# Kernel optimization log

Hardware: AMD Instinct MI355X
Metric: run time of the kernel (lower is better)

Reference implementation:

```python
import jax, jax.numpy as jnp
import numpy as np

N = 4096
IN_DIM = 512
NUM_HEADS = 8
SUB_DIM = 64
ETA = 0.5
LAMBDA_SPARSE = 0.1
EDGE_PROB = 0.01


def setup_inputs() -> dict:
    key = jax.random.key(0)
    k_h, k_u, k_a = jax.random.split(key, 3)
    H = jax.random.normal(k_h, (N, IN_DIM), dtype=jnp.float32)
    # Per-head orthonormal subspace bases (QR init, as in the torch module)
    raw = jax.random.normal(k_u, (NUM_HEADS, IN_DIM, SUB_DIM), dtype=jnp.float32)
    U = jax.vmap(lambda a: jnp.linalg.qr(a)[0])(raw)  # [K, in_dim, r]
    # Binary adjacency mask with self-loops (float 0/1)
    adj = (jax.random.uniform(k_a, (N, N)) < EDGE_PROB).astype(jnp.float32)
    adj_mask = jnp.maximum(adj, jnp.eye(N, dtype=jnp.float32))
    threshold = jnp.full((IN_DIM,), LAMBDA_SPARSE, dtype=jnp.float32)
    return {"H": H, "adj_mask": adj_mask, "U": U, "threshold": threshold}


def reference(H, adj_mask, U, threshold):
    r = U.shape[-1]
    scale = jnp.asarray(r, H.dtype) ** 0.5
    # Z_k = U_k^T H^T  -> [K, r, n]
    Z = jnp.einsum('kdr,nd->krn', U, H)
    # scores[k, i, j] = Z_k[:, i] . Z_k[:, j] / sqrt(r), masked to neighbors
    scores = jnp.einsum('kri,krj->kij', Z, Z) / scale
    scores = scores + (1.0 - adj_mask) * (-1e9)
    alpha = jax.nn.softmax(scores, axis=-1)          # [K, n, n]
    # Z_agg[k, :, i] = sum_j alpha[k, i, j] * Z_k[:, j]
    Z_agg = jnp.einsum('krj,kij->kri', Z, alpha)      # [K, r, n]
    # project back and sum heads: [n, d]
    agg = jnp.einsum('kdr,kri->id', U, Z_agg)
    H_half = H + ETA * agg
    H_out = jax.nn.relu(H_half - threshold[None, :])
    # orthogonality loss: sum_{k<l} ||U_k^T U_l||_F^2
    gram = jnp.einsum('kdr,lds->klrs', U, U)
    sq = jnp.sum(gram ** 2, axis=(-1, -2))            # [K, K]
    orth_loss = 0.5 * (jnp.sum(sq) - jnp.trace(sq))
    return H_out, orth_loss
```

## Files before the change

kernel.cpp:

```cpp
#include <hip/hip_runtime.h>
#include <hip/hip_bf16.h>

#define NN   4096
#define DD   512
#define KH   8
#define RR   64
#define CAP  128

typedef unsigned short u16;
typedef unsigned int   u32;
typedef __attribute__((ext_vector_type(8))) short short8;
typedef __attribute__((ext_vector_type(4))) float f32x4;

__device__ __forceinline__ float bflo(u32 v){ union{u32 i; float f;} c; c.i = v << 16;        return c.f; }
__device__ __forceinline__ float bfhi(u32 v){ union{u32 i; float f;} c; c.i = v & 0xFFFF0000u; return c.f; }
__device__ __forceinline__ u16 f2bf(float f){ __hip_bfloat16 h = __float2bfloat16(f); return *reinterpret_cast<u16*>(&h); }

__global__ __launch_bounds__(256) void prep_scan(const float* __restrict__ H, const float* __restrict__ U,
                                                 const float* __restrict__ adj,
                                                 u16* __restrict__ Hb, u16* __restrict__ Bt1,
                                                 u16* __restrict__ Bt2,
                                                 int* __restrict__ nlist, int* __restrict__ cnt,
                                                 float* __restrict__ lossA, int* __restrict__ doneA) {
    __shared__ float tile[64][65];
    __shared__ int   list[CAP];
    __shared__ int   cntS;
    const int b = blockIdx.x, t = threadIdx.x;
    if (b < 4096) {
        const int i = b;
        if (t == 0) cntS = 0;
        __syncthreads();
        const float* arow = adj + (size_t)i * NN;
        #pragma unroll
        for (int qq = 0; qq < 4; qq++) {
            int j = (qq * 256 + t) * 4;
            float4 mv = *(const float4*)(arow + j);
            if (mv.x != 0.f) { int p = atomicAdd(&cntS, 1); if (p < CAP) list[p] = j;     }
            if (mv.y != 0.f) { int p = atomicAdd(&cntS, 1); if (p < CAP) list[p] = j + 1; }
            if (mv.z != 0.f) { int p = atomicAdd(&cntS, 1); if (p < CAP) list[p] = j + 2; }
            if (mv.w != 0.f) { int p = atomicAdd(&cntS, 1); if (p < CAP) list[p] = j + 3; }
        }
        __syncthreads();
        const int n = min(cntS, CAP);
        if (t < n) nlist[(size_t)i * CAP + t] = list[t];
        if (t == 0) cnt[i] = n;
        return;
    }
    if (b < 6144) {
        size_t id = (size_t)(b - 4096) * 256 + t;
        float4 v = *(const float4*)(H + id * 4);
        ushort4 o; o.x = f2bf(v.x); o.y = f2bf(v.y); o.z = f2bf(v.z); o.w = f2bf(v.w);
        *(ushort4*)(Hb + id * 4) = o;
        return;
    }
    if (b == 6208) { if (t == 0) { lossA[0] = 0.f; doneA[0] = 0; } return; }
    const int b2 = b - 6144;
    const int k = b2 >> 3, d0 = (b2 & 7) * 64;
    #pragma unroll
    for (int s = 0; s < 4; s++) {
        int u = t + 256 * s;
        int dd = u >> 4, rq = u & 15;
        float4 v = *(const float4*)(U + ((size_t)(k * DD + d0 + dd)) * RR + rq * 4);
        tile[dd][rq * 4 + 0] = v.x; tile[dd][rq * 4 + 1] = v.y;
        tile[dd][rq * 4 + 2] = v.z; tile[dd][rq * 4 + 3] = v.w;
    }
    __syncthreads();
    {   int r = t >> 2;
        #pragma unroll
        for (int ii = 0; ii < 16; ii++) {
            int dd = (t & 3) * 16 + ii;
            Bt1[(size_t)(k * RR + r) * DD + d0 + dd] = f2bf(tile[dd][r]);
        }
    }
    {   int dd = t >> 2, rb = (t & 3) * 16;
        #pragma unroll
        for (int ii = 0; ii < 16; ii++) {
            Bt2[(size_t)(d0 + dd) * DD + k * RR + rb + ii] = f2bf(tile[dd][rb + ii]);
        }
    }
}

__global__ __launch_bounds__(256) void zgemm_mfma(const u16* __restrict__ Hb, const u16* __restrict__ Bt1,
                                                  u16* __restrict__ Zb) {
    __shared__ short As[64][72];
    __shared__ short Bs[64][72];
    const int t = threadIdx.x;
    const int i0 = blockIdx.x * 64, n0 = blockIdx.y * 64;
    const int w = t >> 6, lane = t & 63;
    const int lm = lane & 15, lg = lane >> 4;
    f32x4 acc[4] = {};
    for (int kc = 0; kc < DD; kc += 64) {
        #pragma unroll
        for (int s = 0; s < 2; s++) {
            int c = t + 256 * s; int row = c >> 3, g = c & 7;
            *(short8*)&As[row][g * 8] = *(const short8*)(Hb  + (size_t)(i0 + row) * DD + kc + g * 8);
            *(short8*)&Bs[row][g * 8] = *(const short8*)(Bt1 + (size_t)(n0 + row) * DD + kc + g * 8);
        }
        __syncthreads();
        #pragma unroll
        for (int ks = 0; ks < 64; ks += 32) {
            short8 af = *(const short8*)&As[w * 16 + lm][ks + lg * 8];
            #pragma unroll
            for (int b = 0; b < 4; b++) {
                short8 bfr = *(const short8*)&Bs[b * 16 + lm][ks + lg * 8];
                acc[b] = __builtin_amdgcn_mfma_f32_16x16x32_bf16(af, bfr, acc[b], 0, 0, 0);
            }
        }
        __syncthreads();
    }
    #pragma unroll
    for (int b = 0; b < 4; b++)
        #pragma unroll
        for (int q = 0; q < 4; q++) {
            int row = i0 + w * 16 + lg * 4 + q;
            int col = n0 + b * 16 + lm;
            Zb[(size_t)row * DD + col] = f2bf(acc[b][q]);
        }
}

__global__ __launch_bounds__(512) void attn7(const u16* __restrict__ Zb, const int* __restrict__ nlist,
                                             const int* __restrict__ cnt, u16* __restrict__ Zaggb) {
    const int i = blockIdx.x, t = threadIdx.x;
    const int k = t >> 6, lane = t & 63;
    __shared__ int   nbrS[CAP + 16];
    __shared__ float ziS[DD];
    __shared__ u32   zbufU[KH][16][36];
    __shared__ float wS[KH][16];
    const int ci = cnt[i];
    for (int u = t; u < ci; u += 512) nbrS[u] = nlist[(size_t)i * CAP + u];
    if (t < 256) {
        u32 v = *(const u32*)(Zb + (size_t)i * DD + t * 2);
        ziS[t * 2] = bflo(v); ziS[t * 2 + 1] = bfhi(v);
    }
    __syncthreads();
    if (t < 16) nbrS[ci + t] = nbrS[0];
    __syncthreads();

    const int n = lane >> 2, q = lane & 3;
    const int half = lane >> 5, L = lane & 31;
    const float4* zi4 = (const float4*)(ziS + k * 64 + q * 16);
    float m = -3.0e38f, l = 0.f, accA = 0.f, accB = 0.f;

    for (int base = 0; base < ci; base += 16) {
        const int cact = min(16, ci - base);
        const int j = nbrS[base + n];
        const uint4* zp = (const uint4*)(Zb + (size_t)j * DD + k * 64 + q * 16);
        uint4 v0 = zp[0], v1 = zp[1];
        *(uint4*)&zbufU[k][n][q * 8]     = v0;
        *(uint4*)&zbufU[k][n][q * 8 + 4] = v1;
        float4 a0 = zi4[0], a1 = zi4[1], a2 = zi4[2], a3 = zi4[3];
        float s = bflo(v0.x)*a0.x + bfhi(v0.x)*a0.y + bflo(v0.y)*a0.z + bfhi(v0.y)*a0.w
                + bflo(v0.z)*a1.x + bfhi(v0.z)*a1.y + bflo(v0.w)*a1.z + bfhi(v0.w)*a1.w
                + bflo(v1.x)*a2.x + bfhi(v1.x)*a2.y + bflo(v1.y)*a2.z + bfhi(v1.y)*a2.w
                + bflo(v1.z)*a3.x + bfhi(v1.z)*a3.y + bflo(v1.w)*a3.z + bfhi(v1.w)*a3.w;
        s += __shfl_xor(s, 1);
        s += __shfl_xor(s, 2);
        s *= 0.125f;
        if (n >= cact) s = -3.0e38f;
        float mx = s;
        #pragma unroll
        for (int off = 4; off < 64; off <<= 1) mx = fmaxf(mx, __shfl_xor(mx, off));
        const float mnew = fmaxf(m, mx);
        const float scale = __expf(m - mnew);
        const float e = (n < cact) ? __expf(s - mnew) : 0.f;
        float se = e;
        #pragma unroll
        for (int off = 4; off < 64; off <<= 1) se += __shfl_xor(se, off);
        l = l * scale + se;
        m = mnew;
        accA *= scale; accB *= scale;
        if (q == 0) wS[k][n] = e;
        __syncthreads();
        for (int c = half; c < cact; c += 2) {
            const float wgt = wS[k][c];
            u32 z2 = zbufU[k][c][L];
            accA += wgt * bflo(z2);
            accB += wgt * bfhi(z2);
        }
        __syncthreads();
    }
    accA += __shfl_xor(accA, 32);
    accB += __shfl_xor(accB, 32);
    if (lane < 32) {
        const float inv = 1.0f / l;
        u32 o = ((u32)f2bf(accA * inv)) | (((u32)f2bf(accB * inv)) << 16);
        *(u32*)(Zaggb + (size_t)i * DD + k * 64 + 2 * L) = o;
    }
}

__global__ __launch_bounds__(256) void outgemm_mfma(const u16* __restrict__ Ab, const u16* __restrict__ Btb,
                                                    const float* __restrict__ H, const float* __restrict__ thr,
                                                    float* __restrict__ out) {
    __shared__ short As[64][72];
    __shared__ short Bs[64][72];
    const int t = threadIdx.x;
    const int i0 = blockIdx.x * 64, n0 = blockIdx.y * 64;
    const int w = t >> 6, lane = t & 63;
    const int lm = lane & 15, lg = lane >> 4;
    f32x4 acc[4] = {};
    for (int kc = 0; kc < DD; kc += 64) {
        #pragma unroll
        for (int s = 0; s < 2; s++) {
            int c = t + 256 * s; int row = c >> 3, g = c & 7;
            *(short8*)&As[row][g * 8] = *(const short8*)(Ab  + (size_t)(i0 + row) * DD + kc + g * 8);
            *(short8*)&Bs[row][g * 8] = *(const short8*)(Btb + (size_t)(n0 + row) * DD + kc + g * 8);
        }
        __syncthreads();
        #pragma unroll
        for (int ks = 0; ks < 64; ks += 32) {
            short8 af = *(const short8*)&As[w * 16 + lm][ks + lg * 8];
            #pragma unroll
            for (int b = 0; b < 4; b++) {
                short8 bfr = *(const short8*)&Bs[b * 16 + lm][ks + lg * 8];
                acc[b] = __builtin_amdgcn_mfma_f32_16x16x32_bf16(af, bfr, acc[b], 0, 0, 0);
            }
        }
        __syncthreads();
    }
    #pragma unroll
    for (int b = 0; b < 4; b++) {
        const int col = n0 + b * 16 + lm;
        const float th = thr[col];
        #pragma unroll
        for (int q = 0; q < 4; q++) {
            int row = i0 + w * 16 + lg * 4 + q;
            float h = H[(size_t)row * DD + col];
            out[(size_t)row * DD + col] = fmaxf(h + 0.5f * acc[b][q] - th, 0.f);
        }
    }
}

__global__ __launch_bounds__(256) void orth_kernel(const float* __restrict__ U, float* __restrict__ loss,
                                                   int* __restrict__ done, float* __restrict__ outLoss) {
    __shared__ float UkT[64][20];
    __shared__ float UlT[64][68];
    const int pb = blockIdx.x >> 2, strip = blockIdx.x & 3;
    int idx = pb, k = 0, lh = 1;
    #pragma unroll
    for (int kk = 0; kk < 8; kk++) {
        int c = 7 - kk;
        if (idx < c) { k = kk; lh = kk + 1 + idx; break; }
        idx -= c;
    }
    const int t = threadIdx.x;
    const int r = t & 15;
    const int s0 = (t >> 4) * 4;
    const int r0g = strip * 16;
    const float* Uk = U + (size_t)k  * DD * RR;
    const float* Ul = U + (size_t)lh * DD * RR;
    float a0 = 0.f, a1 = 0.f, a2 = 0.f, a3 = 0.f;
    for (int dc = 0; dc < DD; dc += 64) {
        {   int dd = t >> 2, rq = t & 3;
            *(float4*)&UkT[dd][rq * 4] = *(const float4*)(Uk + (size_t)(dc + dd) * RR + r0g + rq * 4);
        }
        #pragma unroll
        for (int s = 0; s < 4; s++) {
            int u = t + 256 * s;
            int dd = u >> 4, sq = u & 15;
            *(float4*)&UlT[dd][sq * 4] = *(const float4*)(Ul + (size_t)(dc + dd) * RR + sq * 4);
        }
        __syncthreads();
        #pragma unroll 4
        for (int dd = 0; dd < 64; dd++) {
            float a = UkT[dd][r];
            float4 bv = *(const float4*)&UlT[dd][s0];
            a0 += a * bv.x; a1 += a * bv.y; a2 += a * bv.z; a3 += a * bv.w;
        }
        __syncthreads();
    }
    float v = a0 * a0 + a1 * a1 + a2 * a2 + a3 * a3;
    #pragma unroll
    for (int off = 32; off; off >>= 1) v += __shfl_down(v, off, 64);
    __shared__ float red[4];
    if ((t & 63) == 0) red[t >> 6] = v;
    __syncthreads();
    if (t == 0) {
        atomicAdd(loss, red[0] + red[1] + red[2] + red[3]);
        __threadfence();
        int d = atomicAdd(done, 1);
        if (d == 111) {
            float total = atomicAdd(loss, 0.f);
            outLoss[0] = total;
        }
    }
}

extern "C" void kernel_launch(void* const* d_in, const int* in_sizes, int n_in,
                              void* d_out, int out_size, void* d_ws, size_t ws_size,
                              hipStream_t stream) {
    const float* H   = (const float*)d_in[0];
    const float* adj = (const float*)d_in[1];
    const float* U   = (const float*)d_in[2];
    const float* thr = (const float*)d_in[3];
    float* out = (float*)d_out;

    char* ws = (char*)d_ws;
    float* lossA = (float*)ws;
    int*   doneA = (int*)(ws + 64);
    u16*   Hb    = (u16*)(ws + 1024);
    u16*   Zb    = (u16*)(ws + 1024 + 4u * 1024 * 1024);
    u16*   Zaggb = (u16*)(ws + 1024 + 8u * 1024 * 1024);
    u16*   Bt1   = (u16*)(ws + 1024 + 12u * 1024 * 1024);
    u16*   Bt2   = (u16*)(ws + 1024 + 12u * 1024 * 1024 + 512u * 1024);
    int*   nlist = (int*)(ws + 1024 + 13u * 1024 * 1024);
    int*   cnt   = (int*)(ws + 1024 + 15u * 1024 * 1024 + 512u * 1024);

    prep_scan<<<6209, 256, 0, stream>>>(H, U, adj, Hb, Bt1, Bt2, nlist, cnt, lossA, doneA);
    zgemm_mfma<<<dim3(64, 8), 256, 0, stream>>>(Hb, Bt1, Zb);
    attn7<<<NN, 512, 0, stream>>>(Zb, nlist, cnt, Zaggb);
    outgemm_mfma<<<dim3(64, 8), 256, 0, stream>>>(Zaggb, Bt2, H, thr, out);
    orth_kernel<<<112, 256, 0, stream>>>(U, lossA, doneA, out + (size_t)NN * DD);
}
```

Before: 174.9 us.

## Keep attention accumulation in registers and drop shared-memory staging and barriers

The sparse attention kernel no longer stages neighbor rows, weights, query vector and neighbor list in LDS. Each lane keeps its 16-element slice of the query and a 16-float accumulator in registers, rescales it online, and the lanes are combined with a butterfly shuffle reduction once at the end. This removes two __syncthreads per 16-neighbor chunk and the LDS traffic. In exchange it uses more registers and adds a 16-wide shuffle reduction at the end.

```diff
diff --git a/kernel.cpp b/kernel.cpp
--- a/kernel.cpp
+++ b/kernel.cpp
@@ -118,41 +118,41 @@
         }
 }
 
-__global__ __launch_bounds__(512) void attn7(const u16* __restrict__ Zb, const int* __restrict__ nlist,
+__global__ __launch_bounds__(512) void attn8(const u16* __restrict__ Zb, const int* __restrict__ nlist,
                                              const int* __restrict__ cnt, u16* __restrict__ Zaggb) {
     const int i = blockIdx.x, t = threadIdx.x;
     const int k = t >> 6, lane = t & 63;
-    __shared__ int   nbrS[CAP + 16];
-    __shared__ float ziS[DD];
-    __shared__ u32   zbufU[KH][16][36];
-    __shared__ float wS[KH][16];
+    const int n = lane >> 2, q = lane & 3;
     const int ci = cnt[i];
-    for (int u = t; u < ci; u += 512) nbrS[u] = nlist[(size_t)i * CAP + u];
-    if (t < 256) {
-        u32 v = *(const u32*)(Zb + (size_t)i * DD + t * 2);
-        ziS[t * 2] = bflo(v); ziS[t * 2 + 1] = bfhi(v);
-    }
-    __syncthreads();
-    if (t < 16) nbrS[ci + t] = nbrS[0];
-    __syncthreads();
-
-    const int n = lane >> 2, q = lane & 3;
-    const int half = lane >> 5, L = lane & 31;
-    const float4* zi4 = (const float4*)(ziS + k * 64 + q * 16);
-    float m = -3.0e38f, l = 0.f, accA = 0.f, accB = 0.f;
+    const int* nl = nlist + (size_t)i * CAP;
+
+    float a[16];
+    {
+        const uint4* zp = (const uint4*)(Zb + (size_t)i * DD + k * 64 + q * 16);
+        uint4 w0 = zp[0], w1 = zp[1];
+        a[0] = bflo(w0.x); a[1] = bfhi(w0.x); a[2]  = bflo(w0.y); a[3]  = bfhi(w0.y);
+        a[4] = bflo(w0.z); a[5] = bfhi(w0.z); a[6]  = bflo(w0.w); a[7]  = bfhi(w0.w);
+        a[8] = bflo(w1.x); a[9] = bfhi(w1.x); a[10] = bflo(w1.y); a[11] = bfhi(w1.y);
+        a[12]= bflo(w1.z); a[13]= bfhi(w1.z); a[14] = bflo(w1.w); a[15] = bfhi(w1.w);
+    }
+
+    float m = -3.0e38f, l = 0.f;
+    float acc[16] = {};
 
     for (int base = 0; base < ci; base += 16) {
         const int cact = min(16, ci - base);
-        const int j = nbrS[base + n];
+        const int idx = (n < cact) ? base + n : 0;
+        const int j = nl[idx];
         const uint4* zp = (const uint4*)(Zb + (size_t)j * DD + k * 64 + q * 16);
         uint4 v0 = zp[0], v1 = zp[1];
-        *(uint4*)&zbufU[k][n][q * 8]     = v0;
-        *(uint4*)&zbufU[k][n][q * 8 + 4] = v1;
-        float4 a0 = zi4[0], a1 = zi4[1], a2 = zi4[2], a3 = zi4[3];
-        float s = bflo(v0.x)*a0.x + bfhi(v0.x)*a0.y + bflo(v0.y)*a0.z + bfhi(v0.y)*a0.w
-                + bflo(v0.z)*a1.x + bfhi(v0.z)*a1.y + bflo(v0.w)*a1.z + bfhi(v0.w)*a1.w
-                + bflo(v1.x)*a2.x + bfhi(v1.x)*a2.y + bflo(v1.y)*a2.z + bfhi(v1.y)*a2.w
-                + bflo(v1.z)*a3.x + bfhi(v1.z)*a3.y + bflo(v1.w)*a3.z + bfhi(v1.w)*a3.w;
+        float zf[16];
+        zf[0] = bflo(v0.x); zf[1] = bfhi(v0.x); zf[2]  = bflo(v0.y); zf[3]  = bfhi(v0.y);
+        zf[4] = bflo(v0.z); zf[5] = bfhi(v0.z); zf[6]  = bflo(v0.w); zf[7]  = bfhi(v0.w);
+        zf[8] = bflo(v1.x); zf[9] = bfhi(v1.x); zf[10] = bflo(v1.y); zf[11] = bfhi(v1.y);
+        zf[12]= bflo(v1.z); zf[13]= bfhi(v1.z); zf[14] = bflo(v1.w); zf[15] = bfhi(v1.w);
+        float s = 0.f;
+        #pragma unroll
+        for (int d = 0; d < 16; d++) s += zf[d] * a[d];
         s += __shfl_xor(s, 1);
         s += __shfl_xor(s, 2);
         s *= 0.125f;
@@ -168,23 +168,22 @@
         for (int off = 4; off < 64; off <<= 1) se += __shfl_xor(se, off);
         l = l * scale + se;
         m = mnew;
-        accA *= scale; accB *= scale;
-        if (q == 0) wS[k][n] = e;
-        __syncthreads();
-        for (int c = half; c < cact; c += 2) {
-            const float wgt = wS[k][c];
-            u32 z2 = zbufU[k][c][L];
-            accA += wgt * bflo(z2);
-            accB += wgt * bfhi(z2);
-        }
-        __syncthreads();
-    }
-    accA += __shfl_xor(accA, 32);
-    accB += __shfl_xor(accB, 32);
-    if (lane < 32) {
+        #pragma unroll
+        for (int d = 0; d < 16; d++) acc[d] = acc[d] * scale + e * zf[d];
+    }
+    #pragma unroll
+    for (int off = 4; off < 64; off <<= 1)
+        #pragma unroll
+        for (int d = 0; d < 16; d++) acc[d] += __shfl_xor(acc[d], off);
+    if (n == 0) {
         const float inv = 1.0f / l;
-        u32 o = ((u32)f2bf(accA * inv)) | (((u32)f2bf(accB * inv)) << 16);
-        *(u32*)(Zaggb + (size_t)i * DD + k * 64 + 2 * L) = o;
+        u32 o[8];
+        #pragma unroll
+        for (int p = 0; p < 8; p++)
+            o[p] = ((u32)f2bf(acc[2 * p] * inv)) | (((u32)f2bf(acc[2 * p + 1] * inv)) << 16);
+        uint4* dst = (uint4*)(Zaggb + (size_t)i * DD + k * 64 + q * 16);
+        dst[0] = make_uint4(o[0], o[1], o[2], o[3]);
+        dst[1] = make_uint4(o[4], o[5], o[6], o[7]);
     }
 }
 
@@ -307,7 +306,7 @@
 
     prep_scan<<<6209, 256, 0, stream>>>(H, U, adj, Hb, Bt1, Bt2, nlist, cnt, lossA, doneA);
     zgemm_mfma<<<dim3(64, 8), 256, 0, stream>>>(Hb, Bt1, Zb);
-    attn7<<<NN, 512, 0, stream>>>(Zb, nlist, cnt, Zaggb);
+    attn8<<<NN, 512, 0, stream>>>(Zb, nlist, cnt, Zaggb);
     outgemm_mfma<<<dim3(64, 8), 256, 0, stream>>>(Zaggb, Bt2, H, thr, out);
     orth_kernel<<<112, 256, 0, stream>>>(U, lossA, doneA, out + (size_t)NN * DD);
 }
```

Measured after the change: 181.0 us. 3.5% more time.
